# Kernel optimization log

Hardware: AMD Instinct MI355X
Metric: run time of the kernel (lower is better)

## Reference

```python
import jax, jax.numpy as jnp
import numpy as np

GROUPS = 3
EPS = 1e-5

def _conv(x, w, groups, pad):
    # x: NCHW, w: OIHW (grouped). pad: 'VALID' for 1x1, ((1,1),(1,1)) for 3x3 same.
    return jax.lax.conv_general_dilated(
        x, w, window_strides=(1, 1), padding=pad,
        feature_group_count=groups,
        dimension_numbers=('NCHW', 'OIHW', 'NCHW'))

def _bn(x, g, b, m, v):
    # folded inference batchnorm: y = x*scale + (beta - mean*scale)
    s = g / jnp.sqrt(v + EPS)
    return x * s[None, :, None, None] + (b - m * s)[None, :, None, None]

def _shuffle(x, groups):
    B, C, H, W = x.shape
    return x.reshape(B, groups, C // groups, H, W).transpose(0, 2, 1, 3, 4).reshape(B, C, H, W)

def setup_inputs() -> dict:
    key = jax.random.key(0)
    ks = jax.random.split(key, 16)
    B, Cin, Cout, H, W = 64, 480, 480, 28, 28
    mid = Cout // 4  # 120
    d = {}
    d['x'] = jax.random.normal(ks[0], (B, Cin, H, W), jnp.float32)
    d['w1'] = jax.random.normal(ks[1], (mid, Cin // GROUPS, 1, 1), jnp.float32) * 0.05
    d['g1'] = jax.random.uniform(ks[2], (mid,), jnp.float32)
    d['b1'] = jax.random.normal(ks[3], (mid,), jnp.float32)
    d['m1'] = jax.random.normal(ks[4], (mid,), jnp.float32)
    d['v1'] = jax.random.uniform(ks[5], (mid,), jnp.float32)
    d['w2'] = jax.random.normal(ks[6], (mid, 1, 3, 3), jnp.float32) * 0.05
    d['g2'] = jax.random.uniform(ks[7], (mid,), jnp.float32)
    d['b2'] = jax.random.normal(ks[8], (mid,), jnp.float32)
    d['m2'] = jax.random.normal(ks[9], (mid,), jnp.float32)
    d['v2'] = jax.random.uniform(ks[10], (mid,), jnp.float32)
    d['w3'] = jax.random.normal(ks[11], (Cout, mid // GROUPS, 1, 1), jnp.float32) * 0.05
    d['g3'] = jax.random.uniform(ks[12], (Cout,), jnp.float32)
    d['b3'] = jax.random.normal(ks[13], (Cout,), jnp.float32)
    d['m3'] = jax.random.normal(ks[14], (Cout,), jnp.float32)
    d['v3'] = jax.random.uniform(ks[15], (Cout,), jnp.float32)
    return d

def reference(x, w1, g1, b1, m1, v1, w2, g2, b2, m2, v2, w3, g3, b3, m3, v3):
    mid = w2.shape[0]
    shortcut = x  # in_channels == out_channels -> identity shortcut
    out = jax.nn.relu(_bn(_conv(x, w1, GROUPS, 'VALID'), g1, b1, m1, v1))
    out = _bn(_conv(out, w2, mid, ((1, 1), (1, 1))), g2, b2, m2, v2)  # depthwise 3x3
    out = _shuffle(out, GROUPS)
    out = jax.nn.relu(_bn(_conv(out, w3, GROUPS, 'VALID'), g3, b3, m3, v3))
    return out + shortcut
```

## Files before the change

### kernel.cpp

```cpp
#include <hip/hip_runtime.h>


namespace {
constexpr int CIN = 480;
constexpr int MID = 120;
constexpr int HWP = 784;
constexpr float EPSV = 1e-5f;

constexpr size_t TMP1_N   = (size_t)64 * MID * HWP;
constexpr size_t G_SHORTS = (size_t)784 * 3 * 4096;
constexpr size_t G_FLOATS = G_SHORTS / 2;
constexpr size_t PAR_OFF  = TMP1_N + G_FLOATS;
constexpr int WA1_N = 3 * 3 * 5 * 64 * 8;
constexpr int WA3_N = 3 * 10 * 2 * 64 * 8;

constexpr int S1X = 168;
constexpr int S1O = 65;
constexpr int S2O = 69;
constexpr int S3O = 67;
}

typedef short bf16x8 __attribute__((ext_vector_type(8)));
typedef float f32x4  __attribute__((ext_vector_type(4)));

__device__ inline unsigned short f2bf(float v) {
    unsigned u = __float_as_uint(v);
    return (unsigned short)((u + 0x7fffu + ((u >> 16) & 1u)) >> 16);
}
__device__ inline float bf2f(unsigned s) {
    return __uint_as_float(s << 16);
}
__device__ inline void split2(float v, unsigned short& h, unsigned short& l) {
    h = f2bf(v);
    l = f2bf(v - bf2f(h));
}

__global__ __launch_bounds__(256) void prep_k(
    const float* __restrict__ w1, const float* __restrict__ w3,
    const float* __restrict__ g1, const float* __restrict__ b1,
    const float* __restrict__ m1, const float* __restrict__ v1,
    const float* __restrict__ g2, const float* __restrict__ b2,
    const float* __restrict__ m2, const float* __restrict__ v2,
    const float* __restrict__ g3, const float* __restrict__ b3,
    const float* __restrict__ m3, const float* __restrict__ v3,
    float* __restrict__ par, unsigned short* __restrict__ wpk)
{
    const int t = blockIdx.x * 256 + threadIdx.x;
    if (t < 720) {
        if (t < 120) {
            const float s = g1[t] * rsqrtf(v1[t] + EPSV);
            par[t] = s; par[120 + t] = fmaf(-m1[t], s, b1[t]);
        } else if (t < 240) {
            const int c = t - 120;
            const float s = g2[c] * rsqrtf(v2[c] + EPSV);
            par[240 + c] = s; par[360 + c] = fmaf(-m2[c], s, b2[c]);
        } else {
            const int c = t - 240;
            const float s = g3[c] * rsqrtf(v3[c] + EPSV);
            par[480 + c] = s; par[960 + c] = fmaf(-m3[c], s, b3[c]);
        }
    } else if (t < 3600) {
        const int t1   = t - 720;
        const int lane = t1 & 63;
        const int rest = t1 >> 6;
        const int ks   = rest % 5;
        const int mtg  = rest / 5;
        const int mt   = mtg % 3;
        const int g    = mtg / 3;
        const int row  = mt * 16 + (lane & 15);
        const int k0   = ks * 32 + (lane >> 4) * 8;
        unsigned short h[8], l[8];
#pragma unroll
        for (int j = 0; j < 8; ++j) {
            float v = (row < 40) ? w1[(size_t)(g * 40 + row) * 160 + k0 + j] : 0.f;
            split2(v, h[j], l[j]);
        }
        *reinterpret_cast<uint4*>(wpk + (size_t)t1 * 8)         = *reinterpret_cast<uint4*>(h);
        *reinterpret_cast<uint4*>(wpk + WA1_N + (size_t)t1 * 8) = *reinterpret_cast<uint4*>(l);
    } else if (t < 7440) {
        const int t3   = t - 3600;
        const int lane = t3 & 63;
        const int rest = t3 >> 6;
        const int ks   = rest % 2;
        const int mtg  = rest / 2;
        const int mt   = mtg % 10;
        const int g    = mtg / 10;
        const int row  = mt * 16 + (lane & 15);
        const int k0   = ks * 32 + (lane >> 4) * 8;
        unsigned short h[8], l[8];
#pragma unroll
        for (int j = 0; j < 8; ++j) {
            const int k = k0 + j;
            float v = (k < 40) ? w3[(size_t)(g * 160 + row) * 40 + k] : 0.f;
            split2(v, h[j], l[j]);
        }
        *reinterpret_cast<uint4*>(wpk + 2 * WA1_N + (size_t)t3 * 8)         = *reinterpret_cast<uint4*>(h);
        *reinterpret_cast<uint4*>(wpk + 2 * WA1_N + WA3_N + (size_t)t3 * 8) = *reinterpret_cast<uint4*>(l);
    }
}

__global__ __launch_bounds__(256) void k1_mfma(
    const float* __restrict__ x, const unsigned short* __restrict__ wA1h,
    const float* __restrict__ par, unsigned short* __restrict__ tmp1)
{
    __shared__ __align__(16) unsigned short xs[64 * S1X];
    __shared__ float sL[40], shL[40];

    const int tid  = threadIdx.x;
    const int lane = tid & 63;
    const int wv   = tid >> 6;
    const int g    = blockIdx.y;
    const int p0   = blockIdx.x * 64;

    if (tid < 40) { sL[tid] = par[g * 40 + tid]; shL[tid] = par[120 + g * 40 + tid]; }

    float4 v[10];
#pragma unroll
    for (int i = 0; i < 10; ++i) {
        const int task = tid + i * 256;
        const int ch   = task >> 4;
        const int px4  = task & 15;
        const int p    = p0 + px4 * 4;
        const int b    = p / HWP;
        const int hw   = p - b * HWP;
        v[i] = *reinterpret_cast<const float4*>(
            x + ((size_t)b * CIN + g * 160 + ch) * HWP + hw);
    }
#pragma unroll
    for (int i = 0; i < 10; ++i) {
        const int task = tid + i * 256;
        const int ch   = task >> 4;
        const int px4  = task & 15;
        unsigned short* d = xs + (px4 * 4) * S1X + ch;
        d[0]       = f2bf(v[i].x);
        d[S1X]     = f2bf(v[i].y);
        d[2 * S1X] = f2bf(v[i].z);
        d[3 * S1X] = f2bf(v[i].w);
    }
    __syncthreads();

    const unsigned short* __restrict__ wA1l = wA1h + WA1_N;
    f32x4 acc[3];
#pragma unroll
    for (int mt = 0; mt < 3; ++mt) acc[mt] = f32x4{0.f, 0.f, 0.f, 0.f};

    const int n16 = lane & 15;
    const int kq  = lane >> 4;
    const int pxl = wv * 16 + n16;
#pragma unroll
    for (int ks = 0; ks < 5; ++ks) {
        const bf16x8 Bv = *reinterpret_cast<const bf16x8*>(
            &xs[pxl * S1X + ks * 32 + kq * 8]);
#pragma unroll
        for (int mt = 0; mt < 3; ++mt) {
            const size_t fi = (((size_t)(g * 3 + mt) * 5 + ks) * 64 + lane) * 8;
            const bf16x8 Ah = *reinterpret_cast<const bf16x8*>(wA1h + fi);
            const bf16x8 Al = *reinterpret_cast<const bf16x8*>(wA1l + fi);
            acc[mt] = __builtin_amdgcn_mfma_f32_16x16x32_bf16(Ah, Bv, acc[mt], 0, 0, 0);
            acc[mt] = __builtin_amdgcn_mfma_f32_16x16x32_bf16(Al, Bv, acc[mt], 0, 0, 0);
        }
    }
    __syncthreads();

    float* osr = reinterpret_cast<float*>(xs);
    {
#pragma unroll
        for (int mt = 0; mt < 3; ++mt) {
#pragma unroll
            for (int r = 0; r < 4; ++r) {
                const int ocl = mt * 16 + kq * 4 + r;
                if (ocl < 40) {
                    float val = fmaf(acc[mt][r], sL[ocl], shL[ocl]);
                    osr[ocl * S1O + pxl] = val > 0.f ? val : 0.f;
                }
            }
        }
    }
    __syncthreads();

#pragma unroll
    for (int i = 0; i < 3; ++i) {
        const int task = tid + i * 256;
        if (task < 640) {
            const int ocl = task >> 4;
            const int px4 = task & 15;
            const int p   = p0 + px4 * 4;
            const int b   = p / HWP;
            const int hw  = p - b * HWP;
            const float* s = osr + ocl * S1O + px4 * 4;
            const unsigned lo = (unsigned)f2bf(s[0]) | ((unsigned)f2bf(s[1]) << 16);
            const unsigned hi = (unsigned)f2bf(s[2]) | ((unsigned)f2bf(s[3]) << 16);
            *reinterpret_cast<uint2*>(
                tmp1 + ((size_t)b * MID + g * 40 + ocl) * HWP + hw) = make_uint2(lo, hi);
        }
    }
}

__global__ __launch_bounds__(256) void k2_dw(
    const unsigned short* __restrict__ tmp1, const float* __restrict__ w2,
    const float* __restrict__ par, unsigned short* __restrict__ G)
{
    __shared__ float dout[MID * S2O];
    __shared__ float w2s[1080];
    __shared__ float s2s[120], sh2s[120];

    const int tid = threadIdx.x;
    const int bx  = blockIdx.x;
    const int p0  = bx * 64;

#pragma unroll
    for (int i = 0; i < 3; ++i) {
        const int task = tid + i * 256;
        if (task < 576) {
            const int gk  = task / 192;
            const int off = task - gk * 192;
            *reinterpret_cast<uint4*>(G + ((size_t)bx * 3 + gk) * 4096 + 2560 + (size_t)off * 8) =
                make_uint4(0u, 0u, 0u, 0u);
        }
    }

    for (int i = tid; i < 1080; i += 256) w2s[i] = w2[i];
    if (tid < 120) { s2s[tid] = par[240 + tid]; sh2s[tid] = par[360 + tid]; }
    __syncthreads();

#pragma unroll
    for (int i = 0; i < 8; ++i) {
        const int task = tid + i * 256;
        if (task < 1920) {
            const int ch  = task >> 4;
            const int px4 = task & 15;
            const int p   = p0 + px4 * 4;
            const int b   = p / HWP;
            const int hw  = p - b * HWP;
            const int h   = hw / 28, w = hw - h * 28;
            const unsigned short* __restrict__ in = tmp1 + ((size_t)b * MID + ch) * HWP;
            const float* wk = w2s + ch * 9;

            float a0 = 0.f, a1 = 0.f, a2 = 0.f, a3 = 0.f;
#pragma unroll
            for (int dh = -1; dh <= 1; ++dh) {
                const int hh = h + dh;
                if (hh < 0 || hh > 27) continue;
                const unsigned short* r = in + hh * 28 + w;
                const uint2 cc = *reinterpret_cast<const uint2*>(r);
                const float c0 = bf2f(cc.x & 0xffffu), c1 = bf2f(cc.x >> 16);
                const float c2 = bf2f(cc.y & 0xffffu), c3 = bf2f(cc.y >> 16);
                const float cl = (w > 0)  ? bf2f(r[-1]) : 0.f;
                const float cr = (w < 24) ? bf2f(r[4])  : 0.f;
                const float* wr = wk + (dh + 1) * 3;
                a0 = fmaf(cl, wr[0], a0); a0 = fmaf(c0, wr[1], a0); a0 = fmaf(c1, wr[2], a0);
                a1 = fmaf(c0, wr[0], a1); a1 = fmaf(c1, wr[1], a1); a1 = fmaf(c2, wr[2], a1);
                a2 = fmaf(c1, wr[0], a2); a2 = fmaf(c2, wr[1], a2); a2 = fmaf(c3, wr[2], a2);
                a3 = fmaf(c2, wr[0], a3); a3 = fmaf(c3, wr[1], a3); a3 = fmaf(cr, wr[2], a3);
            }
            const float s  = s2s[ch];
            const float sh = sh2s[ch];
            const int gi = ch / 40;
            const int cs = (ch - gi * 40) * 3 + gi;
            float* d = dout + cs * S2O + px4 * 4;
            d[0] = fmaf(a0, s, sh); d[1] = fmaf(a1, s, sh);
            d[2] = fmaf(a2, s, sh); d[3] = fmaf(a3, s, sh);
        }
    }
    __syncthreads();

#pragma unroll
    for (int i = 0; i < 4; ++i) {
        const int task = tid + i * 256;
        if (task < 960) {
            const int cb  = task >> 6;
            const int pxl = task & 63;
            const int cs0 = cb * 8;
            unsigned short res[8];
#pragma unroll
            for (int j = 0; j < 8; ++j)
                res[j] = f2bf(dout[(cs0 + j) * S2O + pxl]);
            const int gk  = cs0 / 40;
            const int icg = cs0 - gk * 40;
            const int kb8 = icg >> 3, ks = kb8 >> 2, kbl = kb8 & 3;
            const int nt  = pxl >> 4, n16 = pxl & 15;
            unsigned short* dst = G +
                (((((size_t)bx * 3 + gk) * 2 + ks) * 4 + kbl) * 4 + nt) * 128 + n16 * 8;
            *reinterpret_cast<uint4*>(dst) = *reinterpret_cast<uint4*>(res);
        }
    }
}

__global__ __launch_bounds__(256) void k3_mfma(
    const unsigned short* __restrict__ G, const unsigned short* __restrict__ wA3h,
    const float* __restrict__ par,
    const float* __restrict__ x, float* __restrict__ out)
{
    __shared__ float osr[80 * S3O];
    __shared__ float sL[80], shL[80];

    const int tid  = threadIdx.x;
    const int lane = tid & 63;
    const int wv   = tid >> 6;
    const int bx   = blockIdx.x;
    const int g    = blockIdx.y >> 1;
    const int mh   = blockIdx.y & 1;
    if (tid < 80) {
        sL[tid]  = par[480 + g * 160 + mh * 80 + tid];
        shL[tid] = par[960 + g * 160 + mh * 80 + tid];
    }
    __syncthreads();

    const unsigned short* __restrict__ wA3l = wA3h + WA3_N;
    const int nt = wv;
    f32x4 acc[5];
#pragma unroll
    for (int mt = 0; mt < 5; ++mt) acc[mt] = f32x4{0.f, 0.f, 0.f, 0.f};

    const int kbl = lane >> 4, n16l = lane & 15;
#pragma unroll
    for (int ks = 0; ks < 2; ++ks) {
        const bf16x8 Bv = *reinterpret_cast<const bf16x8*>(
            G + (((((size_t)bx * 3 + g) * 2 + ks) * 4 + kbl) * 4 + nt) * 128 + n16l * 8);
#pragma unroll
        for (int mt = 0; mt < 5; ++mt) {
            const size_t fi = (((size_t)(g * 10 + mh * 5 + mt) * 2 + ks) * 64 + lane) * 8;
            const bf16x8 Ah = *reinterpret_cast<const bf16x8*>(wA3h + fi);
            const bf16x8 Al = *reinterpret_cast<const bf16x8*>(wA3l + fi);
            acc[mt] = __builtin_amdgcn_mfma_f32_16x16x32_bf16(Ah, Bv, acc[mt], 0, 0, 0);
            acc[mt] = __builtin_amdgcn_mfma_f32_16x16x32_bf16(Al, Bv, acc[mt], 0, 0, 0);
        }
    }

    {
        const int n16 = lane & 15, kq = lane >> 4;
        const int pxl = nt * 16 + n16;
#pragma unroll
        for (int mt = 0; mt < 5; ++mt) {
#pragma unroll
            for (int r = 0; r < 4; ++r) {
                const int ocl = mt * 16 + kq * 4 + r;
                float val = fmaf(acc[mt][r], sL[ocl], shL[ocl]);
                osr[ocl * S3O + pxl] = val > 0.f ? val : 0.f;
            }
        }
    }
    __syncthreads();

#pragma unroll
    for (int i = 0; i < 5; ++i) {
        const int task = tid + i * 256;
        const int ocl  = task >> 4;
        const int px4  = task & 15;
        const int p    = bx * 64 + px4 * 4;
        const int b    = p / HWP;
        const int hw   = p - b * HWP;
        const int oc   = g * 160 + mh * 80 + ocl;
        const size_t idx = ((size_t)b * CIN + oc) * HWP + hw;
        const float* s = osr + ocl * S3O + px4 * 4;
        const float4 sc = *reinterpret_cast<const float4*>(x + idx);
        float4 o;
        o.x = s[0] + sc.x; o.y = s[1] + sc.y;
        o.z = s[2] + sc.z; o.w = s[3] + sc.w;
        *reinterpret_cast<float4*>(out + idx) = o;
    }
}

extern "C" void kernel_launch(void* const* d_in, const int* in_sizes, int n_in,
                              void* d_out, int out_size, void* d_ws, size_t ws_size,
                              hipStream_t stream) {
    const float* x  = (const float*)d_in[0];
    const float* w1 = (const float*)d_in[1];
    const float* g1 = (const float*)d_in[2];
    const float* b1 = (const float*)d_in[3];
    const float* m1 = (const float*)d_in[4];
    const float* v1 = (const float*)d_in[5];
    const float* w2 = (const float*)d_in[6];
    const float* g2 = (const float*)d_in[7];
    const float* b2 = (const float*)d_in[8];
    const float* m2 = (const float*)d_in[9];
    const float* v2 = (const float*)d_in[10];
    const float* w3 = (const float*)d_in[11];
    const float* g3 = (const float*)d_in[12];
    const float* b3 = (const float*)d_in[13];
    const float* m3 = (const float*)d_in[14];
    const float* v3 = (const float*)d_in[15];
    float* out = (float*)d_out;

    float* wsf = (float*)d_ws;
    unsigned short* tmp1 = (unsigned short*)wsf;
    unsigned short* G = (unsigned short*)(wsf + TMP1_N);
    float* par = wsf + PAR_OFF;
    unsigned short* wpk = (unsigned short*)(par + 1440);

    prep_k<<<30, 256, 0, stream>>>(w1, w3, g1, b1, m1, v1, g2, b2, m2, v2,
                                   g3, b3, m3, v3, par, wpk);
    k1_mfma<<<dim3(784, 3), 256, 0, stream>>>(x, wpk, par, tmp1);
    k2_dw  <<<784,          256, 0, stream>>>(tmp1, w2, par, G);
    k3_mfma<<<dim3(784, 6), 256, 0, stream>>>(G, wpk + 2 * WA1_N, par, x, out);
}
```

Baseline: 100.4 us.

## Fuse depthwise conv into grouped 1x1 MFMA kernel and pack x staging pairs

The depthwise 3x3 + BN + shuffle stage is merged into the final grouped 1x1 MFMA kernel. Each block computes its group's 40 shuffled channels into shared memory and builds the MFMA B-fragments locally, which removes the global G buffer round trip and one kernel launch. Each block now covers all 160 output channels of a group instead of 80, and the k3 grid shrinks from 784x6 to 784x3 blocks. In k1, pairs of channels are loaded and packed into 32-bit shared writes to cut LDS store count. The cost is larger per-block register and LDS footprint. w2 and the BN parameters are now read straight from global memory rather than staged in LDS.

After: 105.4 us. +5.0%, slower.

```diff
diff --git a/kernel.cpp b/kernel.cpp
--- a/kernel.cpp
+++ b/kernel.cpp
@@ -7,14 +7,11 @@
 constexpr int HWP = 784;
 constexpr float EPSV = 1e-5f;
 
-constexpr size_t TMP1_N   = (size_t)64 * MID * HWP;
-constexpr size_t G_SHORTS = (size_t)784 * 3 * 4096;
-constexpr size_t G_FLOATS = G_SHORTS / 2;
-constexpr size_t PAR_OFF  = TMP1_N + G_FLOATS;
+constexpr size_t TMP1_N = (size_t)64 * MID * HWP;
 constexpr int WA1_N = 3 * 3 * 5 * 64 * 8;
 constexpr int WA3_N = 3 * 10 * 2 * 64 * 8;
 
-constexpr int S1X = 168;
+constexpr int S1W = 84;
 constexpr int S1O = 65;
 constexpr int S2O = 69;
 constexpr int S3O = 67;
@@ -32,7 +29,7 @@
 }
 __device__ inline void split2(float v, unsigned short& h, unsigned short& l) {
     h = f2bf(v);
-    l = f2bf(v - bf2f(h));
+    l = f2bf(v - bf2f((unsigned)h));
 }
 
 __global__ __launch_bounds__(256) void prep_k(
@@ -103,7 +100,7 @@
     const float* __restrict__ x, const unsigned short* __restrict__ wA1h,
     const float* __restrict__ par, unsigned short* __restrict__ tmp1)
 {
-    __shared__ __align__(16) unsigned short xs[64 * S1X];
+    __shared__ __align__(16) unsigned xs32[64 * S1W];
     __shared__ float sL[40], shL[40];
 
     const int tid  = threadIdx.x;
@@ -114,32 +111,34 @@
 
     if (tid < 40) { sL[tid] = par[g * 40 + tid]; shL[tid] = par[120 + g * 40 + tid]; }
 
-    float4 v[10];
-#pragma unroll
-    for (int i = 0; i < 10; ++i) {
-        const int task = tid + i * 256;
-        const int ch   = task >> 4;
-        const int px4  = task & 15;
-        const int p    = p0 + px4 * 4;
-        const int b    = p / HWP;
-        const int hw   = p - b * HWP;
-        v[i] = *reinterpret_cast<const float4*>(
-            x + ((size_t)b * CIN + g * 160 + ch) * HWP + hw);
-    }
-#pragma unroll
-    for (int i = 0; i < 10; ++i) {
-        const int task = tid + i * 256;
-        const int ch   = task >> 4;
-        const int px4  = task & 15;
-        unsigned short* d = xs + (px4 * 4) * S1X + ch;
-        d[0]       = f2bf(v[i].x);
-        d[S1X]     = f2bf(v[i].y);
-        d[2 * S1X] = f2bf(v[i].z);
-        d[3 * S1X] = f2bf(v[i].w);
+    const int px4s = (tid >> 4) & 15;
+    {
+        const int ps = p0 + px4s * 4;
+        const int bs = ps / HWP;
+        const int hws = ps - bs * HWP;
+        const float* __restrict__ xb = x + ((size_t)bs * CIN + g * 160) * HWP + hws;
+
+        float4 v0[5], v1[5];
+#pragma unroll
+        for (int i = 0; i < 5; ++i) {
+            const int cp = (tid & 15) + 16 * i;
+            v0[i] = *reinterpret_cast<const float4*>(xb + (size_t)(2 * cp)     * HWP);
+            v1[i] = *reinterpret_cast<const float4*>(xb + (size_t)(2 * cp + 1) * HWP);
+        }
+#pragma unroll
+        for (int i = 0; i < 5; ++i) {
+            const int cp = (tid & 15) + 16 * i;
+            unsigned* d = xs32 + (px4s * 4) * S1W + cp;
+            d[0]       = (unsigned)f2bf(v0[i].x) | ((unsigned)f2bf(v1[i].x) << 16);
+            d[S1W]     = (unsigned)f2bf(v0[i].y) | ((unsigned)f2bf(v1[i].y) << 16);
+            d[2 * S1W] = (unsigned)f2bf(v0[i].z) | ((unsigned)f2bf(v1[i].z) << 16);
+            d[3 * S1W] = (unsigned)f2bf(v0[i].w) | ((unsigned)f2bf(v1[i].w) << 16);
+        }
     }
     __syncthreads();
 
     const unsigned short* __restrict__ wA1l = wA1h + WA1_N;
+    const unsigned short* xsh = reinterpret_cast<const unsigned short*>(xs32);
     f32x4 acc[3];
 #pragma unroll
     for (int mt = 0; mt < 3; ++mt) acc[mt] = f32x4{0.f, 0.f, 0.f, 0.f};
@@ -150,7 +149,7 @@
 #pragma unroll
     for (int ks = 0; ks < 5; ++ks) {
         const bf16x8 Bv = *reinterpret_cast<const bf16x8*>(
-            &xs[pxl * S1X + ks * 32 + kq * 8]);
+            xsh + pxl * (2 * S1W) + ks * 32 + kq * 8);
 #pragma unroll
         for (int mt = 0; mt < 3; ++mt) {
             const size_t fi = (((size_t)(g * 3 + mt) * 5 + ks) * 64 + lane) * 8;
@@ -162,7 +161,7 @@
     }
     __syncthreads();
 
-    float* osr = reinterpret_cast<float*>(xs);
+    float* osr = reinterpret_cast<float*>(xs32);
     {
 #pragma unroll
         for (int mt = 0; mt < 3; ++mt) {
@@ -196,45 +195,46 @@
     }
 }
 
-__global__ __launch_bounds__(256) void k2_dw(
+__global__ __launch_bounds__(256) void k3_fused(
     const unsigned short* __restrict__ tmp1, const float* __restrict__ w2,
-    const float* __restrict__ par, unsigned short* __restrict__ G)
+    const unsigned short* __restrict__ wA3h, const float* __restrict__ par,
+    const float* __restrict__ x, float* __restrict__ out)
 {
-    __shared__ float dout[MID * S2O];
-    __shared__ float w2s[1080];
-    __shared__ float s2s[120], sh2s[120];
-
-    const int tid = threadIdx.x;
-    const int bx  = blockIdx.x;
-    const int p0  = bx * 64;
+    __shared__ __align__(16) float uni[160 * S3O];
+    __shared__ float sL[160], shL[160];
+
+    float* dout = uni;
+    unsigned short* Bfr = reinterpret_cast<unsigned short*>(uni + 40 * S2O);
+    float* osr = uni;
+
+    const int tid  = threadIdx.x;
+    const int lane = tid & 63;
+    const int wv   = tid >> 6;
+    const int bx   = blockIdx.x;
+    const int gk   = blockIdx.y;
+    const int p0   = bx * 64;
+
+    if (tid < 160) {
+        sL[tid]  = par[480 + gk * 160 + tid];
+        shL[tid] = par[960 + gk * 160 + tid];
+    }
+    if (tid < 192)
+        *reinterpret_cast<uint4*>(Bfr + 2560 + tid * 8) = make_uint4(0u, 0u, 0u, 0u);
 
 #pragma unroll
     for (int i = 0; i < 3; ++i) {
         const int task = tid + i * 256;
-        if (task < 576) {
-            const int gk  = task / 192;
-            const int off = task - gk * 192;
-            *reinterpret_cast<uint4*>(G + ((size_t)bx * 3 + gk) * 4096 + 2560 + (size_t)off * 8) =
-                make_uint4(0u, 0u, 0u, 0u);
-        }
-    }
-
-    for (int i = tid; i < 1080; i += 256) w2s[i] = w2[i];
-    if (tid < 120) { s2s[tid] = par[240 + tid]; sh2s[tid] = par[360 + tid]; }
-    __syncthreads();
-
-#pragma unroll
-    for (int i = 0; i < 8; ++i) {
-        const int task = tid + i * 256;
-        if (task < 1920) {
-            const int ch  = task >> 4;
+        if (task < 640) {
+            const int csl = task >> 4;
             const int px4 = task & 15;
+            const int cs  = gk * 40 + csl;
+            const int c   = (cs % 3) * 40 + cs / 3;
             const int p   = p0 + px4 * 4;
             const int b   = p / HWP;
             const int hw  = p - b * HWP;
             const int h   = hw / 28, w = hw - h * 28;
-            const unsigned short* __restrict__ in = tmp1 + ((size_t)b * MID + ch) * HWP;
-            const float* wk = w2s + ch * 9;
+            const unsigned short* __restrict__ in = tmp1 + ((size_t)b * MID + c) * HWP;
+            const float* __restrict__ wk = w2 + c * 9;
 
             float a0 = 0.f, a1 = 0.f, a2 = 0.f, a3 = 0.f;
 #pragma unroll
@@ -253,85 +253,64 @@
                 a2 = fmaf(c1, wr[0], a2); a2 = fmaf(c2, wr[1], a2); a2 = fmaf(c3, wr[2], a2);
                 a3 = fmaf(c2, wr[0], a3); a3 = fmaf(c3, wr[1], a3); a3 = fmaf(cr, wr[2], a3);
             }
-            const float s  = s2s[ch];
-            const float sh = sh2s[ch];
-            const int gi = ch / 40;
-            const int cs = (ch - gi * 40) * 3 + gi;
-            float* d = dout + cs * S2O + px4 * 4;
+            const float s  = par[240 + c];
+            const float sh = par[360 + c];
+            float* d = dout + csl * S2O + px4 * 4;
             d[0] = fmaf(a0, s, sh); d[1] = fmaf(a1, s, sh);
             d[2] = fmaf(a2, s, sh); d[3] = fmaf(a3, s, sh);
         }
     }
     __syncthreads();
 
-#pragma unroll
-    for (int i = 0; i < 4; ++i) {
-        const int task = tid + i * 256;
-        if (task < 960) {
-            const int cb  = task >> 6;
-            const int pxl = task & 63;
-            const int cs0 = cb * 8;
-            unsigned short res[8];
-#pragma unroll
-            for (int j = 0; j < 8; ++j)
-                res[j] = f2bf(dout[(cs0 + j) * S2O + pxl]);
-            const int gk  = cs0 / 40;
-            const int icg = cs0 - gk * 40;
-            const int kb8 = icg >> 3, ks = kb8 >> 2, kbl = kb8 & 3;
-            const int nt  = pxl >> 4, n16 = pxl & 15;
-            unsigned short* dst = G +
-                (((((size_t)bx * 3 + gk) * 2 + ks) * 4 + kbl) * 4 + nt) * 128 + n16 * 8;
-            *reinterpret_cast<uint4*>(dst) = *reinterpret_cast<uint4*>(res);
-        }
-    }
-}
-
-__global__ __launch_bounds__(256) void k3_mfma(
-    const unsigned short* __restrict__ G, const unsigned short* __restrict__ wA3h,
-    const float* __restrict__ par,
-    const float* __restrict__ x, float* __restrict__ out)
-{
-    __shared__ float osr[80 * S3O];
-    __shared__ float sL[80], shL[80];
-
-    const int tid  = threadIdx.x;
-    const int lane = tid & 63;
-    const int wv   = tid >> 6;
-    const int bx   = blockIdx.x;
-    const int g    = blockIdx.y >> 1;
-    const int mh   = blockIdx.y & 1;
-    if (tid < 80) {
-        sL[tid]  = par[480 + g * 160 + mh * 80 + tid];
-        shL[tid] = par[960 + g * 160 + mh * 80 + tid];
+    {
+        const int task = tid;
+#pragma unroll
+        for (int i = 0; i < 2; ++i) {
+            const int t2 = task + i * 256;
+            if (t2 < 320) {
+                const int cb  = t2 >> 6;
+                const int pxl = t2 & 63;
+                unsigned short res[8];
+#pragma unroll
+                for (int j = 0; j < 8; ++j)
+                    res[j] = f2bf(dout[(cb * 8 + j) * S2O + pxl]);
+                const int ks = cb >> 2, kbl = cb & 3;
+                const int nt = pxl >> 4, n16 = pxl & 15;
+                *reinterpret_cast<uint4*>(
+                    Bfr + (((ks * 4 + kbl) * 4 + nt) * 16 + n16) * 8) =
+                    *reinterpret_cast<uint4*>(res);
+            }
+        }
     }
     __syncthreads();
 
     const unsigned short* __restrict__ wA3l = wA3h + WA3_N;
-    const int nt = wv;
-    f32x4 acc[5];
-#pragma unroll
-    for (int mt = 0; mt < 5; ++mt) acc[mt] = f32x4{0.f, 0.f, 0.f, 0.f};
-
-    const int kbl = lane >> 4, n16l = lane & 15;
+    f32x4 acc[10];
+#pragma unroll
+    for (int mt = 0; mt < 10; ++mt) acc[mt] = f32x4{0.f, 0.f, 0.f, 0.f};
+
+    const int kbl = lane >> 4, n16 = lane & 15;
+    const int nt  = wv;
 #pragma unroll
     for (int ks = 0; ks < 2; ++ks) {
         const bf16x8 Bv = *reinterpret_cast<const bf16x8*>(
-            G + (((((size_t)bx * 3 + g) * 2 + ks) * 4 + kbl) * 4 + nt) * 128 + n16l * 8);
-#pragma unroll
-        for (int mt = 0; mt < 5; ++mt) {
-            const size_t fi = (((size_t)(g * 10 + mh * 5 + mt) * 2 + ks) * 64 + lane) * 8;
+            Bfr + (((ks * 4 + kbl) * 4 + nt) * 16 + n16) * 8);
+#pragma unroll
+        for (int mt = 0; mt < 10; ++mt) {
+            const size_t fi = (((size_t)(gk * 10 + mt) * 2 + ks) * 64 + lane) * 8;
             const bf16x8 Ah = *reinterpret_cast<const bf16x8*>(wA3h + fi);
             const bf16x8 Al = *reinterpret_cast<const bf16x8*>(wA3l + fi);
             acc[mt] = __builtin_amdgcn_mfma_f32_16x16x32_bf16(Ah, Bv, acc[mt], 0, 0, 0);
             acc[mt] = __builtin_amdgcn_mfma_f32_16x16x32_bf16(Al, Bv, acc[mt], 0, 0, 0);
         }
     }
+    __syncthreads();
 
     {
-        const int n16 = lane & 15, kq = lane >> 4;
+        const int kq = lane >> 4;
         const int pxl = nt * 16 + n16;
 #pragma unroll
-        for (int mt = 0; mt < 5; ++mt) {
+        for (int mt = 0; mt < 10; ++mt) {
 #pragma unroll
             for (int r = 0; r < 4; ++r) {
                 const int ocl = mt * 16 + kq * 4 + r;
@@ -343,14 +322,14 @@
     __syncthreads();
 
 #pragma unroll
-    for (int i = 0; i < 5; ++i) {
+    for (int i = 0; i < 10; ++i) {
         const int task = tid + i * 256;
         const int ocl  = task >> 4;
         const int px4  = task & 15;
-        const int p    = bx * 64 + px4 * 4;
+        const int p    = p0 + px4 * 4;
         const int b    = p / HWP;
         const int hw   = p - b * HWP;
-        const int oc   = g * 160 + mh * 80 + ocl;
+        const int oc   = gk * 160 + ocl;
         const size_t idx = ((size_t)b * CIN + oc) * HWP + hw;
         const float* s = osr + ocl * S3O + px4 * 4;
         const float4 sc = *reinterpret_cast<const float4*>(x + idx);
@@ -384,13 +363,11 @@
 
     float* wsf = (float*)d_ws;
     unsigned short* tmp1 = (unsigned short*)wsf;
-    unsigned short* G = (unsigned short*)(wsf + TMP1_N);
-    float* par = wsf + PAR_OFF;
+    float* par = wsf + TMP1_N / 2;
     unsigned short* wpk = (unsigned short*)(par + 1440);
 
     prep_k<<<30, 256, 0, stream>>>(w1, w3, g1, b1, m1, v1, g2, b2, m2, v2,
                                    g3, b3, m3, v3, par, wpk);
     k1_mfma<<<dim3(784, 3), 256, 0, stream>>>(x, wpk, par, tmp1);
-    k2_dw  <<<784,          256, 0, stream>>>(tmp1, w2, par, G);
-    k3_mfma<<<dim3(784, 6), 256, 0, stream>>>(G, wpk + 2 * WA1_N, par, x, out);
-}
+    k3_fused<<<dim3(784, 3), 256, 0, stream>>>(tmp1, w2, wpk + 2 * WA1_N, par, x, out);
+}
```
